# Performance work log

Hardware: AMD Instinct MI355X
Metric: run time of the kernel (lower is better)

Reference implementation:

```python
import jax, jax.numpy as jnp
import numpy as np

B, F, H = 128, 12288, 2048   # batch, flattened-image dim (3x64x64), MLP hidden
TAU = 0.1                    # constraint(x) = relu(x@W1)@w2 - TAU  (so constraint(0) = -TAU < 0)
THRESHOLD = 1e-3
MAX_STEPS = 30


def setup_inputs() -> dict:
    key = jax.random.key(0)
    k1, k2, k3 = jax.random.split(key, 3)
    x0 = jnp.zeros((B, F), jnp.float32)                 # anchor point, constraint(x0) < 0 by construction
    x = jax.random.normal(k1, (B, F), jnp.float32)
    W1 = jax.random.normal(k2, (F, H), jnp.float32) / np.float32(np.sqrt(F))
    w2 = jax.random.normal(k3, (H,), jnp.float32) / np.float32(np.sqrt(H))
    return {"x0": x0, "x": x, "W1": W1, "w2": w2}


def reference(x0, x, W1, w2):
    def fvals(c):  # per-sample constraint value at interpolation coeff c: [B]
        xc = (1.0 - c)[:, None] * x0 + c[:, None] * x
        return jax.nn.relu(xc @ W1) @ w2 - TAU

    # f(0) = -TAU < 0 (asserted in original). Check f(1): samples already feasible skip search.
    f1 = fvals(jnp.ones((B,), jnp.float32))
    inside = f1 <= 0.0

    a = jnp.zeros((B,), jnp.float32)
    b = jnp.ones((B,), jnp.float32)
    c = jnp.ones((B,), jnp.float32)
    done = inside  # feasible samples keep c = 1 (projected == x)

    def step(carry, _):
        a, b, c, done = carry
        cm = (a + b) * 0.5
        v = fvals(cm)
        upd = ~done
        hit = upd & (v >= -THRESHOLD) & (v < 0.0)   # -threshold <= f(c) < 0 -> converged
        go_a = upd & (v < 0.0) & ~hit               # same sign as f(a): move a
        go_b = upd & (v >= 0.0)                     # opposite sign: move b
        a = jnp.where(go_a, cm, a)
        b = jnp.where(go_b, cm, b)
        c = jnp.where(upd, cm, c)                   # freeze c once done
        done = done | hit
        return (a, b, c, done), None

    (a, b, c, done), _ = jax.lax.scan(step, (a, b, c, done), None, length=MAX_STEPS)

    c = jnp.where(inside, 1.0, c)
    proj = (1.0 - c)[:, None] * x0 + c[:, None] * x
    # Original raises ConvergenceError -> NaN fill for non-converged samples.
    return jnp.where(done[:, None], proj, jnp.float32(jnp.nan))
```

## Files before the change

kernel.cpp:

```cpp
#include <hip/hip_runtime.h>
#include <hip/hip_bf16.h>

#define BB 128
#define FF 12288
#define HH 2048
#define TAU_F 0.1f
#define THR_F 1e-3f
#define NKG (FF / 8)
#define BH (BB * HH)
#define NFLAGS 192
#define SKD 16

typedef __attribute__((ext_vector_type(4))) float f32x4;
typedef __attribute__((ext_vector_type(8))) short s16x8;
typedef __attribute__((ext_vector_type(8))) unsigned short u16x8;

__device__ __forceinline__ void barrier_lds() {
    asm volatile("s_waitcnt lgkmcnt(0)\ns_barrier" ::: "memory");
}

__device__ __forceinline__ void bsplit(float v, unsigned short& h, unsigned short& l) {
    unsigned int u  = __float_as_uint(v);
    unsigned int rh = (u + 0x7fffu + ((u >> 16) & 1u)) >> 16;
    float hf = __uint_as_float(rh << 16);
    float lf = v - hf;
    unsigned int ul = __float_as_uint(lf);
    unsigned int rl = (ul + 0x7fffu + ((ul >> 16) & 1u)) >> 16;
    h = (unsigned short)rh;
    l = (unsigned short)rl;
}

__device__ __forceinline__ bool read_nz(const int* __restrict__ flags) {
    const int lane = threadIdx.x & 63;
    int v = 0;
    if (lane < NFLAGS / 4) {
        const int4 q = ((const int4*)flags)[lane];
        v = q.x | q.y | q.z | q.w;
    }
    return __any(v != 0);
}

__device__ __forceinline__ void presplit_blk(
    const float* __restrict__ X, unsigned short* __restrict__ AH,
    unsigned short* __restrict__ AL, int i, int t) {
    const int kg = i * 8 + (t & 7);
#pragma unroll
    for (int r = 0; r < 4; ++r) {
        const int m = (t >> 3) + r * 32;
        const float* src = X + (size_t)m * FF + kg * 8;
        u16x8 hv, lv;
#pragma unroll
        for (int j = 0; j < 8; ++j) {
            unsigned short h, lo;
            bsplit(src[j], h, lo);
            hv[j] = h; lv[j] = lo;
        }
        const size_t o = ((size_t)kg * BB + m) * 8;
        *(u16x8*)(AH + o) = hv;
        *(u16x8*)(AL + o) = lv;
    }
}

__global__ __launch_bounds__(256) void presplit_kernel(
    const float* __restrict__ x, const float* __restrict__ x0,
    unsigned short* __restrict__ Ah, unsigned short* __restrict__ Al,
    int* __restrict__ flags) {
    const int z = blockIdx.y;
    const int i = blockIdx.x;
    const int t = threadIdx.x;
    if (z == 0) {
        presplit_blk(x, Ah, Al, i, t);
        return;
    }
    __shared__ int snz[4];
    const int w = t >> 6, lane = t & 63;
    const int kg = i * 8 + (t & 7);
    int tnz = 0;
#pragma unroll
    for (int r = 0; r < 4; ++r) {
        const int m = (t >> 3) + r * 32;
        const float4* src = (const float4*)(x0 + (size_t)m * FF + kg * 8);
        const float4 a = src[0], b = src[1];
        tnz |= (a.x != 0.f) | (a.y != 0.f) | (a.z != 0.f) | (a.w != 0.f)
             | (b.x != 0.f) | (b.y != 0.f) | (b.z != 0.f) | (b.w != 0.f);
    }
    const int wnz = __any(tnz != 0) ? 1 : 0;
    if (lane == 0) snz[w] = wnz;
    __syncthreads();
    const int bnz = snz[0] | snz[1] | snz[2] | snz[3];
    if (t == 0) flags[i] = bnz;
    if (bnz) {
        const size_t zoff = (size_t)NKG * BB * 8;
        presplit_blk(x0, Ah + zoff, Al + zoff, i, t);
    }
}

__global__ __launch_bounds__(256, 2) void mfma_gemm_kernel(
    const unsigned short* __restrict__ Ah, const unsigned short* __restrict__ Al,
    const float* __restrict__ W1, float* __restrict__ P,
    const int* __restrict__ flags, int SK, int KC, int NIT) {
    const int z = blockIdx.y;
    if (z == 1 && !read_nz(flags)) return;

    const int nwg = gridDim.x;
    const int bx  = blockIdx.x;
    const int wg  = (bx & 7) * (nwg >> 3) + (bx >> 3);
    const int ct  = wg & 31;
    const int kc  = wg >> 5;

    const int t   = threadIdx.x;
    const int w   = t >> 6;
    const int l   = t & 63;
    const int kgl = l >> 4;
    const int li  = l & 15;

    __shared__ unsigned short lds[2][4096];

    const size_t zoffA = (size_t)z * NKG * BB * 8;
    const unsigned short* APH = Ah + zoffA;
    const unsigned short* APL = Al + zoffA;
    const bool zchk = (z == 1);

    f32x4 acc[2][4];
#pragma unroll
    for (int mt = 0; mt < 2; ++mt)
#pragma unroll
        for (int nt = 0; nt < 4; ++nt) acc[mt][nt] = (f32x4)0.f;

    const int kbase = kc * KC;
    const int kg0   = kbase >> 3;
    const int bkg = t >> 6;
    const int bn  = t & 63;

    s16x8 ahE[2], alE[2], ahO[2], alO[2];
    auto loadA = [&](s16x8* ah, s16x8* al, int it) {
        const int kg = kg0 + it * 4 + kgl;
        if (zchk && flags[kg >> 3] == 0) {
#pragma unroll
            for (int mt = 0; mt < 2; ++mt) { ah[mt] = (s16x8)0; al[mt] = (s16x8)0; }
            return;
        }
#pragma unroll
        for (int mt = 0; mt < 2; ++mt) {
            const size_t o = ((size_t)kg * BB + w * 32 + mt * 16 + li) * 8;
            ah[mt] = *(const s16x8*)(APH + o);
            al[mt] = *(const s16x8*)(APL + o);
        }
    };

    auto stageB_load = [&](int it, float* v) {
        const float* src = W1 + (size_t)(kbase + it * 32 + bkg * 8) * HH + ct * 64 + bn;
#pragma unroll
        for (int j = 0; j < 8; ++j) v[j] = src[(size_t)j * HH];
    };
    auto stageB_write = [&](int buf, const float* v) {
        u16x8 hv, lv;
#pragma unroll
        for (int j = 0; j < 8; ++j) {
            unsigned short h, lo;
            bsplit(v[j], h, lo);
            hv[j] = h; lv[j] = lo;
        }
        unsigned short* d = &lds[buf][(bkg * 64 + bn) * 8];
        *(u16x8*)(d)        = hv;
        *(u16x8*)(d + 2048) = lv;
    };
    auto computeR = [&](const s16x8* ah, const s16x8* al, int buf) {
        const unsigned short* L = lds[buf];
#pragma unroll
        for (int nt = 0; nt < 4; ++nt) {
            const int no = (kgl * 64 + nt * 16 + li) * 8;
            const s16x8 fbh = *(const s16x8*)&L[no];
            const s16x8 fbl = *(const s16x8*)&L[2048 + no];
#pragma unroll
            for (int mt = 0; mt < 2; ++mt) {
                acc[mt][nt] = __builtin_amdgcn_mfma_f32_16x16x32_bf16(ah[mt], fbh, acc[mt][nt], 0, 0, 0);
                acc[mt][nt] = __builtin_amdgcn_mfma_f32_16x16x32_bf16(ah[mt], fbl, acc[mt][nt], 0, 0, 0);
                acc[mt][nt] = __builtin_amdgcn_mfma_f32_16x16x32_bf16(al[mt], fbh, acc[mt][nt], 0, 0, 0);
            }
        }
    };

    float bvE[8], bvO[8];
    loadA(ahE, alE, 0);
    stageB_load(0, bvE);
    stageB_write(0, bvE);
    if (NIT > 1) stageB_load(1, bvO);
    barrier_lds();

    for (int it = 0; it < NIT; it += 2) {
        const bool m1 = (it + 1 < NIT);
        const bool m2 = (it + 2 < NIT);
        const bool m3 = (it + 3 < NIT);
        if (m2) stageB_load(it + 2, bvE);
        if (m1) loadA(ahO, alO, it + 1);
        computeR(ahE, alE, 0);
        if (m1) stageB_write(1, bvO);
        barrier_lds();
        if (m1) {
            if (m3) stageB_load(it + 3, bvO);
            if (m2) loadA(ahE, alE, it + 2);
            computeR(ahO, alO, 1);
            if (m2) stageB_write(0, bvE);
            barrier_lds();
        }
    }

    float* dst = P + (size_t)(z * SK + kc) * BH;
    const int r0 = w * 32 + (l >> 4) * 4;
    const int c0 = ct * 64 + li;
#pragma unroll
    for (int mt = 0; mt < 2; ++mt)
#pragma unroll
        for (int nt = 0; nt < 4; ++nt)
#pragma unroll
            for (int r = 0; r < 4; ++r)
                dst[(size_t)(r0 + mt * 16 + r) * HH + c0 + nt * 16] = acc[mt][nt][r];
}

__device__ __forceinline__ void solve_linear(float S, float& c, bool& done) {
    const bool inside = (S - TAU_F <= 0.f);
    float a = 0.f, bh = 1.f;
    c = 1.f; done = inside;
    for (int it = 0; it < 30; ++it) {
        const float cm = 0.5f * (a + bh);
        const float v = cm * S - TAU_F;
        const bool upd  = !done;
        const bool hit  = upd && (v >= -THR_F) && (v < 0.f);
        const bool go_a = upd && (v < 0.f) && !hit;
        const bool go_b = upd && (v >= 0.f);
        a  = go_a ? cm : a;
        bh = go_b ? cm : bh;
        c  = upd  ? cm : c;
        done = done || hit;
    }
    c = inside ? 1.f : c;
}

__global__ __launch_bounds__(1024) void bisect_write_kernel(
    const float* __restrict__ P, const float* __restrict__ w2,
    const float* __restrict__ x, const float* __restrict__ x0,
    const int* __restrict__ flags, float* __restrict__ out, int SK) {
    const int b = blockIdx.x;
    const int t = threadIdx.x;
    const int w = t >> 6;
    const int lane = t & 63;
    __shared__ float red[16];
    const bool nz = read_nz(flags);

    const float2* P1 = (const float2*)(P + (size_t)b * HH) + t;
    float2 u1 = {0.f, 0.f};
    for (int kc = 0; kc < SK; ++kc) {
        const float2 v = P1[(size_t)kc * (BH / 2)];
        u1.x += v.x; u1.y += v.y;
    }
    const float2 wv = ((const float2*)w2)[t];

    auto blockReduce = [&](float v) -> float {
#pragma unroll
        for (int off = 32; off > 0; off >>= 1) v += __shfl_xor(v, off);
        if (lane == 0) red[w] = v;
        __syncthreads();
        float s = 0.f;
#pragma unroll
        for (int i = 0; i < 16; ++i) s += red[i];
        __syncthreads();
        return s;
    };

    float c = 1.f;
    bool done = false;
    if (!nz) {
        float p = fmaf(fmaxf(u1.x, 0.f), wv.x, fmaxf(u1.y, 0.f) * wv.y);
        const float S = blockReduce(p);
        solve_linear(S, c, done);
    } else {
        const float2* P0 = (const float2*)(P + (size_t)(SK * BH) + (size_t)b * HH) + t;
        float2 u0 = {0.f, 0.f};
        for (int kc = 0; kc < SK; ++kc) {
            const float2 v = P0[(size_t)kc * (BH / 2)];
            u0.x += v.x; u0.y += v.y;
        }
        const float2 dd = {u1.x - u0.x, u1.y - u0.y};
        auto feval = [&](float cc) -> float {
            float p = fmaf(fmaxf(fmaf(cc, dd.x, u0.x), 0.f), wv.x,
                           fmaxf(fmaf(cc, dd.y, u0.y), 0.f) * wv.y);
            return blockReduce(p) - TAU_F;
        };
        const float f1 = feval(1.f);
        const bool inside = (f1 <= 0.f);
        float a = 0.f, bh = 1.f;
        done = inside;
        for (int it = 0; it < 30; ++it) {
            const float cm = 0.5f * (a + bh);
            const float v = feval(cm);
            const bool upd  = !done;
            const bool hit  = upd && (v >= -THR_F) && (v < 0.f);
            const bool go_a = upd && (v < 0.f) && !hit;
            const bool go_b = upd && (v >= 0.f);
            a  = go_a ? cm : a;
            bh = go_b ? cm : bh;
            c  = upd  ? cm : c;
            done = done || hit;
        }
        c = inside ? 1.f : c;
    }

    const float nanv = __int_as_float(0x7fc00000);
    const float4* xr  = (const float4*)(x  + (size_t)b * FF);
    const float4* x0r = (const float4*)(x0 + (size_t)b * FF);
    float4* orow = (float4*)(out + (size_t)b * FF);
    if (!done) {
        float4 o; o.x = o.y = o.z = o.w = nanv;
#pragma unroll
        for (int k2 = 0; k2 < 3; ++k2) orow[t + 1024 * k2] = o;
    } else if (!nz) {
#pragma unroll
        for (int k2 = 0; k2 < 3; ++k2) {
            const int i = t + 1024 * k2;
            float4 xv = xr[i], o;
            o.x = c * xv.x; o.y = c * xv.y; o.z = c * xv.z; o.w = c * xv.w;
            orow[i] = o;
        }
    } else {
#pragma unroll
        for (int k2 = 0; k2 < 3; ++k2) {
            const int i = t + 1024 * k2;
            float4 xv = xr[i], zv = x0r[i], o;
            o.x = fmaf(c, xv.x - zv.x, zv.x);
            o.y = fmaf(c, xv.y - zv.y, zv.y);
            o.z = fmaf(c, xv.z - zv.z, zv.z);
            o.w = fmaf(c, xv.w - zv.w, zv.w);
            orow[i] = o;
        }
    }
}

__global__ __launch_bounds__(256) void zflags_kernel(
    const float4* __restrict__ x0, int* __restrict__ flags) {
    const int t = threadIdx.x;
    const int w = t >> 6, lane = t & 63;
    __shared__ int snz[4];
    int tnz = 0;
    const int base = blockIdx.x * 2048 + t;
#pragma unroll
    for (int j = 0; j < 8; ++j) {
        float4 v = x0[base + 256 * j];
        tnz |= (v.x != 0.f) | (v.y != 0.f) | (v.z != 0.f) | (v.w != 0.f);
    }
    const int wnz = __any(tnz != 0) ? 1 : 0;
    if (lane == 0) snz[w] = wnz;
    __syncthreads();
    if (t == 0) flags[blockIdx.x] = snz[0] | snz[1] | snz[2] | snz[3];
}

__global__ __launch_bounds__(256) void legacy_gemm_kernel(
    const float* __restrict__ x, const float* __restrict__ x0,
    const float* __restrict__ W1, float* __restrict__ P,
    const int* __restrict__ flags) {
    const int ct = blockIdx.x, z = blockIdx.z, t = threadIdx.x;
    if (z == 1 && !read_nz(flags)) return;
    const int cg = t & 7, rg = t >> 3;
    const int r0 = rg * 4, cc = ct * 64 + cg * 8;
    float acc[4][8];
#pragma unroll
    for (int i = 0; i < 4; ++i)
#pragma unroll
        for (int n = 0; n < 8; ++n) acc[i][n] = 0.f;
    const float* __restrict__ X = z ? x0 : x;
    for (int k = 0; k < FF; k += 4) {
        float xr[4][4];
#pragma unroll
        for (int i = 0; i < 4; ++i) {
            float4 v = *(const float4*)(X + (size_t)(r0 + i) * FF + k);
            xr[i][0] = v.x; xr[i][1] = v.y; xr[i][2] = v.z; xr[i][3] = v.w;
        }
        float wr[4][8];
#pragma unroll
        for (int j = 0; j < 4; ++j) {
            float4 a = *(const float4*)(W1 + (size_t)(k + j) * HH + cc);
            float4 b = *(const float4*)(W1 + (size_t)(k + j) * HH + cc + 4);
            wr[j][0] = a.x; wr[j][1] = a.y; wr[j][2] = a.z; wr[j][3] = a.w;
            wr[j][4] = b.x; wr[j][5] = b.y; wr[j][6] = b.z; wr[j][7] = b.w;
        }
#pragma unroll
        for (int j = 0; j < 4; ++j)
#pragma unroll
            for (int i = 0; i < 4; ++i)
#pragma unroll
                for (int n = 0; n < 8; ++n)
                    acc[i][n] = fmaf(xr[i][j], wr[j][n], acc[i][n]);
    }
    float* Pp = P + (size_t)z * BH;
#pragma unroll
    for (int i = 0; i < 4; ++i) {
        float4 o0, o1;
        o0.x = acc[i][0]; o0.y = acc[i][1]; o0.z = acc[i][2]; o0.w = acc[i][3];
        o1.x = acc[i][4]; o1.y = acc[i][5]; o1.z = acc[i][6]; o1.w = acc[i][7];
        *(float4*)(Pp + (size_t)(r0 + i) * HH + cc) = o0;
        *(float4*)(Pp + (size_t)(r0 + i) * HH + cc + 4) = o1;
    }
}

extern "C" void kernel_launch(void* const* d_in, const int* in_sizes, int n_in,
                              void* d_out, int out_size, void* d_ws, size_t ws_size,
                              hipStream_t stream) {
    const float* x0 = (const float*)d_in[0];
    const float* x  = (const float*)d_in[1];
    const float* W1 = (const float*)d_in[2];
    const float* w2 = (const float*)d_in[3];
    float* out = (float*)d_out;
    char* ws = (char*)d_ws;

    const size_t szA   = (size_t)2 * NKG * BB * 8 * sizeof(unsigned short);
    const size_t offAl = szA;
    const size_t offFl = 2 * szA;
    const size_t offP  = offFl + 1024;

    int SK = 0;
    const int cand[5] = {SKD, 8, 4, 2, 1};
    for (int i = 0; i < 5; ++i) {
        const size_t need = offP + (size_t)2 * cand[i] * BH * sizeof(float);
        if (ws_size >= need) { SK = cand[i]; break; }
    }

    if (SK > 0) {
        unsigned short* Ah = (unsigned short*)ws;
        unsigned short* Al = (unsigned short*)(ws + offAl);
        int*   flags = (int*)(ws + offFl);
        float* P     = (float*)(ws + offP);
        const int KC = FF / SK, NIT = KC / 32;

        presplit_kernel<<<dim3(NFLAGS, 2), 256, 0, stream>>>(x, x0, Ah, Al, flags);
        mfma_gemm_kernel<<<dim3(32 * SK, 2), 256, 0, stream>>>(Ah, Al, W1, P, flags, SK, KC, NIT);
        bisect_write_kernel<<<BB, 1024, 0, stream>>>(P, w2, x, x0, flags, out, SK);
    } else {
        float* P     = (float*)ws;
        int*   flags = (int*)(ws + (size_t)2 * BH * sizeof(float));
        zflags_kernel<<<NFLAGS, 256, 0, stream>>>((const float4*)x0, flags);
        legacy_gemm_kernel<<<dim3(32, 1, 2), 256, 0, stream>>>(x, x0, W1, P, flags);
        bisect_write_kernel<<<BB, 1024, 0, stream>>>(P, w2, x, x0, flags, out, 1);
    }
}
```

Baseline: 49.69 us.

## Fuse bf16 hi/lo splitting of activations into the MFMA GEMM A-load

Removes the presplit kernel that wrote hi/lo bf16 copies of x and x0 to workspace. The GEMM now loads fp32 activations directly and splits them in registers, and a lightweight flags kernel only checks x0 for zeros. This saves a kernel pass and the workspace round trip, but each column tile now redoes the split, reads twice the bytes per A element, and loses the per-kgroup zero skip for x0. The legacy fallback path is removed, so the launch returns with no work when the workspace is too small.

```diff
diff --git a/kernel.cpp b/kernel.cpp
--- a/kernel.cpp
+++ b/kernel.cpp
@@ -6,7 +6,6 @@
 #define HH 2048
 #define TAU_F 0.1f
 #define THR_F 1e-3f
-#define NKG (FF / 8)
 #define BH (BB * HH)
 #define NFLAGS 192
 #define SKD 16
@@ -40,67 +39,31 @@
     return __any(v != 0);
 }
 
-__device__ __forceinline__ void presplit_blk(
-    const float* __restrict__ X, unsigned short* __restrict__ AH,
-    unsigned short* __restrict__ AL, int i, int t) {
-    const int kg = i * 8 + (t & 7);
-#pragma unroll
-    for (int r = 0; r < 4; ++r) {
-        const int m = (t >> 3) + r * 32;
-        const float* src = X + (size_t)m * FF + kg * 8;
-        u16x8 hv, lv;
-#pragma unroll
-        for (int j = 0; j < 8; ++j) {
-            unsigned short h, lo;
-            bsplit(src[j], h, lo);
-            hv[j] = h; lv[j] = lo;
-        }
-        const size_t o = ((size_t)kg * BB + m) * 8;
-        *(u16x8*)(AH + o) = hv;
-        *(u16x8*)(AL + o) = lv;
-    }
-}
-
-__global__ __launch_bounds__(256) void presplit_kernel(
-    const float* __restrict__ x, const float* __restrict__ x0,
-    unsigned short* __restrict__ Ah, unsigned short* __restrict__ Al,
-    int* __restrict__ flags) {
-    const int z = blockIdx.y;
-    const int i = blockIdx.x;
+__global__ __launch_bounds__(256) void zflags_kernel(
+    const float4* __restrict__ x0, int* __restrict__ flags) {
     const int t = threadIdx.x;
-    if (z == 0) {
-        presplit_blk(x, Ah, Al, i, t);
-        return;
-    }
+    const int w = t >> 6, lane = t & 63;
     __shared__ int snz[4];
-    const int w = t >> 6, lane = t & 63;
-    const int kg = i * 8 + (t & 7);
     int tnz = 0;
-#pragma unroll
-    for (int r = 0; r < 4; ++r) {
-        const int m = (t >> 3) + r * 32;
-        const float4* src = (const float4*)(x0 + (size_t)m * FF + kg * 8);
-        const float4 a = src[0], b = src[1];
-        tnz |= (a.x != 0.f) | (a.y != 0.f) | (a.z != 0.f) | (a.w != 0.f)
-             | (b.x != 0.f) | (b.y != 0.f) | (b.z != 0.f) | (b.w != 0.f);
+    const int base = blockIdx.x * 2048 + t;
+#pragma unroll
+    for (int j = 0; j < 8; ++j) {
+        float4 v = x0[base + 256 * j];
+        tnz |= (v.x != 0.f) | (v.y != 0.f) | (v.z != 0.f) | (v.w != 0.f);
     }
     const int wnz = __any(tnz != 0) ? 1 : 0;
     if (lane == 0) snz[w] = wnz;
     __syncthreads();
-    const int bnz = snz[0] | snz[1] | snz[2] | snz[3];
-    if (t == 0) flags[i] = bnz;
-    if (bnz) {
-        const size_t zoff = (size_t)NKG * BB * 8;
-        presplit_blk(x0, Ah + zoff, Al + zoff, i, t);
-    }
+    if (t == 0) flags[blockIdx.x] = snz[0] | snz[1] | snz[2] | snz[3];
 }
 
 __global__ __launch_bounds__(256, 2) void mfma_gemm_kernel(
-    const unsigned short* __restrict__ Ah, const unsigned short* __restrict__ Al,
+    const float* __restrict__ x, const float* __restrict__ x0,
     const float* __restrict__ W1, float* __restrict__ P,
     const int* __restrict__ flags, int SK, int KC, int NIT) {
     const int z = blockIdx.y;
     if (z == 1 && !read_nz(flags)) return;
+    const float* __restrict__ X = z ? x0 : x;
 
     const int nwg = gridDim.x;
     const int bx  = blockIdx.x;
@@ -116,11 +79,6 @@
 
     __shared__ unsigned short lds[2][4096];
 
-    const size_t zoffA = (size_t)z * NKG * BB * 8;
-    const unsigned short* APH = Ah + zoffA;
-    const unsigned short* APL = Al + zoffA;
-    const bool zchk = (z == 1);
-
     f32x4 acc[2][4];
 #pragma unroll
     for (int mt = 0; mt < 2; ++mt)
@@ -128,23 +86,27 @@
         for (int nt = 0; nt < 4; ++nt) acc[mt][nt] = (f32x4)0.f;
 
     const int kbase = kc * KC;
-    const int kg0   = kbase >> 3;
     const int bkg = t >> 6;
     const int bn  = t & 63;
 
     s16x8 ahE[2], alE[2], ahO[2], alO[2];
     auto loadA = [&](s16x8* ah, s16x8* al, int it) {
-        const int kg = kg0 + it * 4 + kgl;
-        if (zchk && flags[kg >> 3] == 0) {
-#pragma unroll
-            for (int mt = 0; mt < 2; ++mt) { ah[mt] = (s16x8)0; al[mt] = (s16x8)0; }
-            return;
-        }
+        const int k0 = kbase + it * 32 + kgl * 8;
 #pragma unroll
         for (int mt = 0; mt < 2; ++mt) {
-            const size_t o = ((size_t)kg * BB + w * 32 + mt * 16 + li) * 8;
-            ah[mt] = *(const s16x8*)(APH + o);
-            al[mt] = *(const s16x8*)(APL + o);
+            const int row = w * 32 + mt * 16 + li;
+            const float4* src = (const float4*)(X + (size_t)row * FF + k0);
+            const float4 a = src[0], b = src[1];
+            float vv[8] = {a.x, a.y, a.z, a.w, b.x, b.y, b.z, b.w};
+            u16x8 hv, lv;
+#pragma unroll
+            for (int j = 0; j < 8; ++j) {
+                unsigned short h, lo;
+                bsplit(vv[j], h, lo);
+                hv[j] = h; lv[j] = lo;
+            }
+            ah[mt] = (s16x8)hv;
+            al[mt] = (s16x8)lv;
         }
     };
 
@@ -336,72 +298,6 @@
     }
 }
 
-__global__ __launch_bounds__(256) void zflags_kernel(
-    const float4* __restrict__ x0, int* __restrict__ flags) {
-    const int t = threadIdx.x;
-    const int w = t >> 6, lane = t & 63;
-    __shared__ int snz[4];
-    int tnz = 0;
-    const int base = blockIdx.x * 2048 + t;
-#pragma unroll
-    for (int j = 0; j < 8; ++j) {
-        float4 v = x0[base + 256 * j];
-        tnz |= (v.x != 0.f) | (v.y != 0.f) | (v.z != 0.f) | (v.w != 0.f);
-    }
-    const int wnz = __any(tnz != 0) ? 1 : 0;
-    if (lane == 0) snz[w] = wnz;
-    __syncthreads();
-    if (t == 0) flags[blockIdx.x] = snz[0] | snz[1] | snz[2] | snz[3];
-}
-
-__global__ __launch_bounds__(256) void legacy_gemm_kernel(
-    const float* __restrict__ x, const float* __restrict__ x0,
-    const float* __restrict__ W1, float* __restrict__ P,
-    const int* __restrict__ flags) {
-    const int ct = blockIdx.x, z = blockIdx.z, t = threadIdx.x;
-    if (z == 1 && !read_nz(flags)) return;
-    const int cg = t & 7, rg = t >> 3;
-    const int r0 = rg * 4, cc = ct * 64 + cg * 8;
-    float acc[4][8];
-#pragma unroll
-    for (int i = 0; i < 4; ++i)
-#pragma unroll
-        for (int n = 0; n < 8; ++n) acc[i][n] = 0.f;
-    const float* __restrict__ X = z ? x0 : x;
-    for (int k = 0; k < FF; k += 4) {
-        float xr[4][4];
-#pragma unroll
-        for (int i = 0; i < 4; ++i) {
-            float4 v = *(const float4*)(X + (size_t)(r0 + i) * FF + k);
-            xr[i][0] = v.x; xr[i][1] = v.y; xr[i][2] = v.z; xr[i][3] = v.w;
-        }
-        float wr[4][8];
-#pragma unroll
-        for (int j = 0; j < 4; ++j) {
-            float4 a = *(const float4*)(W1 + (size_t)(k + j) * HH + cc);
-            float4 b = *(const float4*)(W1 + (size_t)(k + j) * HH + cc + 4);
-            wr[j][0] = a.x; wr[j][1] = a.y; wr[j][2] = a.z; wr[j][3] = a.w;
-            wr[j][4] = b.x; wr[j][5] = b.y; wr[j][6] = b.z; wr[j][7] = b.w;
-        }
-#pragma unroll
-        for (int j = 0; j < 4; ++j)
-#pragma unroll
-            for (int i = 0; i < 4; ++i)
-#pragma unroll
-                for (int n = 0; n < 8; ++n)
-                    acc[i][n] = fmaf(xr[i][j], wr[j][n], acc[i][n]);
-    }
-    float* Pp = P + (size_t)z * BH;
-#pragma unroll
-    for (int i = 0; i < 4; ++i) {
-        float4 o0, o1;
-        o0.x = acc[i][0]; o0.y = acc[i][1]; o0.z = acc[i][2]; o0.w = acc[i][3];
-        o1.x = acc[i][4]; o1.y = acc[i][5]; o1.z = acc[i][6]; o1.w = acc[i][7];
-        *(float4*)(Pp + (size_t)(r0 + i) * HH + cc) = o0;
-        *(float4*)(Pp + (size_t)(r0 + i) * HH + cc + 4) = o1;
-    }
-}
-
 extern "C" void kernel_launch(void* const* d_in, const int* in_sizes, int n_in,
                               void* d_out, int out_size, void* d_ws, size_t ws_size,
                               hipStream_t stream) {
@@ -412,33 +308,20 @@
     float* out = (float*)d_out;
     char* ws = (char*)d_ws;
 
-    const size_t szA   = (size_t)2 * NKG * BB * 8 * sizeof(unsigned short);
-    const size_t offAl = szA;
-    const size_t offFl = 2 * szA;
-    const size_t offP  = offFl + 1024;
+    int* flags = (int*)ws;
+    float* P   = (float*)(ws + 1024);
 
     int SK = 0;
     const int cand[5] = {SKD, 8, 4, 2, 1};
     for (int i = 0; i < 5; ++i) {
-        const size_t need = offP + (size_t)2 * cand[i] * BH * sizeof(float);
+        const size_t need = 1024 + (size_t)2 * cand[i] * BH * sizeof(float);
         if (ws_size >= need) { SK = cand[i]; break; }
     }
-
-    if (SK > 0) {
-        unsigned short* Ah = (unsigned short*)ws;
-        unsigned short* Al = (unsigned short*)(ws + offAl);
-        int*   flags = (int*)(ws + offFl);
-        float* P     = (float*)(ws + offP);
-        const int KC = FF / SK, NIT = KC / 32;
-
-        presplit_kernel<<<dim3(NFLAGS, 2), 256, 0, stream>>>(x, x0, Ah, Al, flags);
-        mfma_gemm_kernel<<<dim3(32 * SK, 2), 256, 0, stream>>>(Ah, Al, W1, P, flags, SK, KC, NIT);
-        bisect_write_kernel<<<BB, 1024, 0, stream>>>(P, w2, x, x0, flags, out, SK);
-    } else {
-        float* P     = (float*)ws;
-        int*   flags = (int*)(ws + (size_t)2 * BH * sizeof(float));
-        zflags_kernel<<<NFLAGS, 256, 0, stream>>>((const float4*)x0, flags);
-        legacy_gemm_kernel<<<dim3(32, 1, 2), 256, 0, stream>>>(x, x0, W1, P, flags);
-        bisect_write_kernel<<<BB, 1024, 0, stream>>>(P, w2, x, x0, flags, out, 1);
-    }
-}
+    if (SK == 0) return;
+
+    const int KC = FF / SK, NIT = KC / 32;
+
+    zflags_kernel<<<NFLAGS, 256, 0, stream>>>((const float4*)x0, flags);
+    mfma_gemm_kernel<<<dim3(32 * SK, 2), 256, 0, stream>>>(x, x0, W1, P, flags, SK, KC, NIT);
+    bisect_write_kernel<<<BB, 1024, 0, stream>>>(P, w2, x, x0, flags, out, SK);
+}
```

After: 68.46 us. 1.38x slower.
